# Kernel tuning notes

Measured on AMD Instinct MI355X. Metric: run time of the kernel, lower is better.

The kernel has to match this reference:

```python
import jax, jax.numpy as jnp
import numpy as np

B = 8192       # batch
HID = 1024     # hidden_dim
HEADS = 8      # head_count
OBS, ACT, N_AGENTS = 128, 32, 4
ENC_IN = N_AGENTS * OBS + ACT   # 544
DEC_IN = (N_AGENTS - 1) * ACT   # 96


def _linear(key, fan_in, fan_out):
    k1, k2 = jax.random.split(key)
    lim = 1.0 / np.sqrt(fan_in)
    W = jax.random.uniform(k1, (fan_in, fan_out), minval=-lim, maxval=lim, dtype=jnp.float32)
    b = jax.random.uniform(k2, (fan_out,), minval=-lim, maxval=lim, dtype=jnp.float32)
    return W, b


def setup_inputs() -> dict:
    key = jax.random.key(0)
    ks = jax.random.split(key, 10)
    s = jax.random.normal(ks[0], (B, N_AGENTS * OBS), dtype=jnp.float32)
    a = jax.random.normal(ks[1], (B, N_AGENTS * ACT), dtype=jnp.float32)
    W_enc_in, b_enc_in = _linear(ks[2], ENC_IN, HID)   # encoder_input_fc
    W_dec_in, b_dec_in = _linear(ks[3], DEC_IN, HID)   # decoder_input_fc
    W_eh, b_eh = _linear(ks[4], HID, HID)              # fc_encoder_input
    head_ks = jax.random.split(ks[5], HEADS)
    Wb = [_linear(k, HID, HID) for k in head_ks]       # fc_encoder_heads
    W_heads = jnp.stack([w for w, _ in Wb], axis=0)    # [H, HID, HID]
    b_heads = jnp.stack([b for _, b in Wb], axis=0)    # [H, HID]
    W_dh, b_dh = _linear(ks[6], HID, HID)              # fc_decoder_input
    W1, b1 = _linear(ks[7], HID, HID)                  # fc1
    W2, b2 = _linear(ks[8], HID, 1)                    # fc2
    return {"s": s, "a": a,
            "W_enc_in": W_enc_in, "b_enc_in": b_enc_in,
            "W_dec_in": W_dec_in, "b_dec_in": b_dec_in,
            "W_eh": W_eh, "b_eh": b_eh,
            "W_heads": W_heads, "b_heads": b_heads,
            "W_dh": W_dh, "b_dh": b_dh,
            "W1": W1, "b1": b1, "W2": W2, "b2": b2}


def reference(s, a, W_enc_in, b_enc_in, W_dec_in, b_dec_in, W_eh, b_eh,
              W_heads, b_heads, W_dh, b_dh, W1, b1, W2, b2):
    relu = jax.nn.relu
    # agent id = 0: own action is a[:, :ACT], others' actions are a[:, ACT:]
    enc_input = jnp.concatenate([s, a[:, :ACT]], axis=1) @ W_enc_in + b_enc_in   # [B, HID]
    dec_input = a[:, ACT:] @ W_dec_in + b_dec_in                                 # [B, HID]
    # Attention_ATT_2
    encoder_h = relu(enc_input @ W_eh + b_eh)                                    # [B, HID]
    encoder_heads = relu(jnp.einsum('bd,hde->hbe', encoder_h, W_heads)
                         + b_heads[:, None, :])                                  # [H, B, HID]
    decoder_H = relu(dec_input @ W_dh + b_dh)                                    # [B, HID]
    scores = jnp.einsum('hbd,bd->bh', encoder_heads, decoder_H)                  # [B, H]
    attn = jax.nn.softmax(scores, axis=1)                                        # [B, H]
    context = jnp.einsum('hbd,bh->bd', encoder_heads, attn)                      # [B, HID]
    x = relu(context @ W1 + b1)
    q = x @ W2 + b2                                                              # [B, 1]
    return q
```

## Files before the change

### kernel.cpp

```cpp
#include <hip/hip_runtime.h>
#include <hip/hip_bf16.h>
#include <hip/hip_fp16.h>

#define BATCH   8192
#define HID     1024
#define HEADS   8
#define BC      2048

typedef unsigned int  u32;
typedef unsigned short u16;
typedef __attribute__((ext_vector_type(8))) short bf16x8;
typedef __attribute__((ext_vector_type(4))) float f32x4;

__device__ __forceinline__ u32 pack_hi2(u32 u0, u32 u1) {
    return (u0 >> 16) | (u1 & 0xFFFF0000u);
}
__device__ __forceinline__ void split1(float x, u16& h, u16& l) {
    const u32 u = __float_as_uint(x);
    h = (u16)(u >> 16);
    const float r = x - __uint_as_float(u & 0xFFFF0000u);
    l = (u16)(__float_as_uint(r) >> 16);
}
__device__ __forceinline__ void splitA4(float4 v, uint2& hi, uint2& lo) {
    u32 u0 = __float_as_uint(v.x), u1 = __float_as_uint(v.y),
        u2 = __float_as_uint(v.z), u3 = __float_as_uint(v.w);
    float r0 = v.x - __uint_as_float(u0 & 0xFFFF0000u);
    float r1 = v.y - __uint_as_float(u1 & 0xFFFF0000u);
    float r2 = v.z - __uint_as_float(u2 & 0xFFFF0000u);
    float r3 = v.w - __uint_as_float(u3 & 0xFFFF0000u);
    hi.x = pack_hi2(u0, u1);
    hi.y = pack_hi2(u2, u3);
    lo.x = pack_hi2(__float_as_uint(r0), __float_as_uint(r1));
    lo.y = pack_hi2(__float_as_uint(r2), __float_as_uint(r3));
}

__device__ __forceinline__ void gld16(const u16* g, u16* l) {
    __builtin_amdgcn_global_load_lds(
        (const __attribute__((address_space(1))) u32*)g,
        (__attribute__((address_space(3))) u32*)l, 16, 0, 0);
}

struct WSplitArgs {
    const float* src[6];
    u16* hi[6];
    u16* lo[6];
};

__global__ __launch_bounds__(256) void split_weight_all(WSplitArgs args)
{
    const int z = blockIdx.z;
    int which, zz = 0;
    if (z < 3)       { which = z; }
    else if (z < 11) { which = 3; zz = z - 3; }
    else             { which = z - 7; }
    const int KT = (which == 4) ? 17 : (which == 5 ? 3 : 32);
    const int kt = blockIdx.x;
    if (kt >= KT) return;
    const int K = KT * 32;
    const long long zoff = (long long)zz * K * 1024;
    const float* W  = args.src[which] + zoff;
    u16* hi = args.hi[which] + zoff;
    u16* lo = args.lo[which] + zoff;

    const int n0  = blockIdx.y * 128;
    const int tid = threadIdx.x;
    const int k   = tid >> 3;
    const int ng  = (tid & 7) * 16;
    const float* src = W + (long long)(kt * 32 + k) * 1024 + n0 + ng;
    u16* dh = hi + ((long long)kt * 1024 + n0) * 32 + k;
    u16* dl = lo + ((long long)kt * 1024 + n0) * 32 + k;
#pragma unroll
    for (int t = 0; t < 4; t++) {
        const float4 v = *(const float4*)(src + t * 4);
        u16 h0, l0, h1, l1, h2, l2, h3, l3;
        split1(v.x, h0, l0); split1(v.y, h1, l1);
        split1(v.z, h2, l2); split1(v.w, h3, l3);
        const int nb = (ng + t * 4) * 32;
        dh[nb]      = h0; dl[nb]      = l0;
        dh[nb + 32] = h1; dl[nb + 32] = l1;
        dh[nb + 64] = h2; dl[nb + 64] = l2;
        dh[nb + 96] = h3; dl[nb + 96] = l3;
    }
}

#define MFMA_Q(IB, JB) \
    __builtin_amdgcn_s_setprio(1); \
    _Pragma("unroll") \
    for (int i_ = 0; i_ < 4; i_++) \
        _Pragma("unroll") \
        for (int j_ = 0; j_ < 2; j_++) \
            acc[(IB) + i_][(JB) + j_] = __builtin_amdgcn_mfma_f32_16x16x32_bf16(ah[i_], bh[(JB) + j_], acc[(IB) + i_][(JB) + j_], 0, 0, 0); \
    _Pragma("unroll") \
    for (int i_ = 0; i_ < 4; i_++) \
        _Pragma("unroll") \
        for (int j_ = 0; j_ < 2; j_++) \
            acc[(IB) + i_][(JB) + j_] = __builtin_amdgcn_mfma_f32_16x16x32_bf16(ah[i_], bl[(JB) + j_], acc[(IB) + i_][(JB) + j_], 0, 0, 0); \
    _Pragma("unroll") \
    for (int i_ = 0; i_ < 4; i_++) \
        _Pragma("unroll") \
        for (int j_ = 0; j_ < 2; j_++) \
            acc[(IB) + i_][(JB) + j_] = __builtin_amdgcn_mfma_f32_16x16x32_bf16(al[i_], bh[(JB) + j_], acc[(IB) + i_][(JB) + j_], 0, 0, 0); \
    __builtin_amdgcn_s_setprio(0);

#define SBAR() \
    __builtin_amdgcn_s_barrier(); \
    __builtin_amdgcn_sched_barrier(0);

#define G_GEOM \
    const int tid  = threadIdx.x; \
    const int lane = tid & 63; \
    const int wv   = tid >> 6; \
    const int wm   = wv >> 1, wn = wv & 1; \
    const int fr   = lane & 15; \
    const int fq   = lane >> 4; \
    const int m0   = blockIdx.y * 256; \
    const int n0   = blockIdx.x * 128; \
    const int lro2 = (lane >> 2) * 32 + (((lane & 3) ^ ((lane >> 3) & 3)) * 8); \
    const int fqx2 = (fq ^ ((fr >> 1) & 3)) * 8; \
    const int wrA  = wv * 32; \
    const int wrB  = wv * 16;

#define G_STAGE_A(buf_, t_) { \
    u16* d_ = (buf_); \
    const long long ao_ = abase + (long long)(t_) * astep; \
    gld16(Ahp + ao_ + (long long)wrA * 32 + lro2, d_ + wrA * 32); \
    gld16(Ahp + ao_ + (long long)(wrA + 16) * 32 + lro2, d_ + (wrA + 16) * 32); \
    gld16(Alp + ao_ + (long long)wrA * 32 + lro2, d_ + 8192 + wrA * 32); \
    gld16(Alp + ao_ + (long long)(wrA + 16) * 32 + lro2, d_ + 8192 + (wrA + 16) * 32); }

#define G_STAGE_B(buf_, t_) { \
    u16* d_ = (buf_); \
    const long long bo_ = bbase + (long long)(t_) * 32768; \
    gld16(Bhp + bo_ + (long long)wrB * 32 + lro2, d_ + 16384 + wrB * 32); \
    gld16(Blp + bo_ + (long long)wrB * 32 + lro2, d_ + 20480 + wrB * 32); }

#define G_RD_A(bp_) \
    _Pragma("unroll") \
    for (int i_ = 0; i_ < 4; i_++) { \
        const int off_ = (wm * 64 + i_ * 16 + fr) * 32 + fqx2; \
        ah[i_] = *(const bf16x8*)((bp_) + off_); \
        al[i_] = *(const bf16x8*)((bp_) + 8192 + off_); }

#define G_RD_B(bp_, JB) \
    _Pragma("unroll") \
    for (int j_ = 0; j_ < 2; j_++) { \
        const int off_ = (wn * 64 + ((JB) + j_) * 16 + fr) * 32 + fqx2; \
        bh[(JB) + j_] = *(const bf16x8*)((bp_) + 16384 + off_); \
        bl[(JB) + j_] = *(const bf16x8*)((bp_) + 20480 + off_); }

#define G_LOOP \
    const int KT = K >> 5; \
    const long long astep = (long long)MA * 32; \
    const long long abase = ((long long)moff + m0) * 32; \
    const long long bbase = (long long)n0 * 32; \
    G_STAGE_A(smem, 0); G_STAGE_B(smem, 0); \
    G_STAGE_A(smem + 24576, 1); G_STAGE_B(smem + 24576, 1); \
    asm volatile("s_waitcnt vmcnt(6)" ::: "memory"); \
    SBAR() \
    for (int t = 0; t < KT; t++) { \
        const u16* bp = smem + (t % 3) * 24576; \
        u16* nb = smem + ((t + 2) % 3) * 24576; \
        const bool more = (t + 2 < KT); \
        bf16x8 ah[4], al[4], bh[4], bl[4]; \
        G_RD_A(bp) \
        G_RD_B(bp, 0) \
        if (more) G_STAGE_A(nb, t + 2); \
        __builtin_amdgcn_sched_barrier(0); \
        MFMA_Q(0, 0) \
        SBAR() \
        G_RD_B(bp, 2) \
        if (more) G_STAGE_B(nb, t + 2); \
        __builtin_amdgcn_sched_barrier(0); \
        MFMA_Q(0, 2) \
        if (more) { asm volatile("s_waitcnt vmcnt(6)" ::: "memory"); } \
        else      { asm volatile("s_waitcnt vmcnt(0)" ::: "memory"); } \
        SBAR() \
    }

template <int RELU, int OUTP>
__global__ __launch_bounds__(512, 2) void gemm_fast(
    const u16* __restrict__ Ahp, const u16* __restrict__ Alp, int MA, int moff,
    const u16* __restrict__ Bhp, const u16* __restrict__ Blp,
    const float* __restrict__ bias,
    float* __restrict__ Cf,
    u16* __restrict__ Chp, u16* __restrict__ Clp, int MC,
    int K)
{
    __shared__ alignas(16) u16 smem[3 * 24576];
    G_GEOM

    f32x4 acc[4][4];
#pragma unroll
    for (int i = 0; i < 4; i++)
#pragma unroll
        for (int j = 0; j < 4; j++) acc[i][j] = 0;

    G_LOOP

#pragma unroll
    for (int j = 0; j < 4; j++) {
        const int n = n0 + wn * 64 + j * 16 + fr;
        const float bb = bias[n];
#pragma unroll
        for (int i = 0; i < 4; i++) {
#pragma unroll
            for (int r = 0; r < 4; r++) {
                const int m = m0 + wm * 64 + i * 16 + fq * 4 + r;
                float v = acc[i][j][r] + bb;
                if (RELU) v = fmaxf(v, 0.0f);
                if (OUTP) {
                    u16 h, l;
                    split1(v, h, l);
                    const long long d = ((long long)(n >> 5) * MC + moff + m) * 32 + (n & 31);
                    Chp[d] = h;
                    Clp[d] = l;
                } else {
                    Cf[(long long)m * 1024 + n] = v;
                }
            }
        }
    }
}

#define H_STAGE_A(buf_, t_) { \
    u16* d_ = (buf_); \
    const long long ao_ = abase + (long long)(t_) * astep; \
    gld16(Ahp + ao_ + (long long)wrA * 32 + lro2, d_ + wrA * 32); \
    gld16(Ahp + ao_ + (long long)(wrA + 16) * 32 + lro2, d_ + (wrA + 16) * 32); \
    gld16(Alp + ao_ + (long long)wrA * 32 + lro2, d_ + 8192 + wrA * 32); \
    gld16(Alp + ao_ + (long long)(wrA + 16) * 32 + lro2, d_ + 8192 + (wrA + 16) * 32); }

#define H_STAGE_B(buf_, t_) { \
    u16* d_ = (buf_); \
    const long long bo_ = bbase + (long long)(t_) * 32768; \
    gld16(Bhp + bo_ + (long long)wrA * 32 + lro2, d_ + 16384 + wrA * 32); \
    gld16(Bhp + bo_ + (long long)(wrA + 16) * 32 + lro2, d_ + 16384 + (wrA + 16) * 32); \
    gld16(Blp + bo_ + (long long)wrA * 32 + lro2, d_ + 24576 + wrA * 32); \
    gld16(Blp + bo_ + (long long)(wrA + 16) * 32 + lro2, d_ + 24576 + (wrA + 16) * 32); }

#define H_RD_A(bp_, RB) \
    _Pragma("unroll") \
    for (int i_ = 0; i_ < 4; i_++) { \
        const int off_ = ((RB) + i_ * 16 + fr) * 32 + fqx2; \
        ah[i_] = *(const bf16x8*)((bp_) + off_); \
        al[i_] = *(const bf16x8*)((bp_) + 8192 + off_); }

#define H_RD_B(bp_, JB) \
    _Pragma("unroll") \
    for (int j_ = 0; j_ < 2; j_++) { \
        const int off_ = (wn * 64 + ((JB) + j_) * 16 + fr) * 32 + fqx2; \
        bh[(JB) + j_] = *(const bf16x8*)((bp_) + 16384 + off_); \
        bl[(JB) + j_] = *(const bf16x8*)((bp_) + 24576 + off_); }

__global__ __launch_bounds__(512, 2) void heads_kernel(
    const u16* __restrict__ Ahp, const u16* __restrict__ Alp, int MA, int moff,
    const u16* __restrict__ Whp, const u16* __restrict__ Wlp,
    const float* __restrict__ b_heads,
    const float* __restrict__ decH,
    __half* __restrict__ headsb,
    float* __restrict__ scoresp)
{
    __shared__ alignas(16) u16 smem[2 * 32768];
    __shared__ float scred[4][256];
    const int tid  = threadIdx.x;
    const int lane = tid & 63;
    const int wv   = tid >> 6;
    const int wm   = wv >> 2;
    const int wn   = wv & 3;
    const int fr   = lane & 15;
    const int fq   = lane >> 4;
    const int m0   = blockIdx.y * 256;
    const int n0   = blockIdx.x * 256;
    const int lro2 = (lane >> 2) * 32 + (((lane & 3) ^ ((lane >> 3) & 3)) * 8);
    const int fqx2 = (fq ^ ((fr >> 1) & 3)) * 8;
    const int wrA  = wv * 32;
    const int h = blockIdx.z;
    const u16* Bhp = Whp + (long long)h * 1048576;
    const u16* Blp = Wlp + (long long)h * 1048576;
    const float* bias = b_heads + h * 1024;

    f32x4 acc[8][4];
#pragma unroll
    for (int i = 0; i < 8; i++)
#pragma unroll
        for (int j = 0; j < 4; j++) acc[i][j] = 0;

    const long long astep = (long long)MA * 32;
    const long long abase = ((long long)moff + m0) * 32;
    const long long bbase = (long long)n0 * 32;

    H_STAGE_A(smem, 0);
    H_STAGE_B(smem, 0);
    asm volatile("s_waitcnt vmcnt(0)" ::: "memory");
    SBAR()

    for (int t = 0; t < 32; t++) {
        const u16* bp = smem + (t & 1) * 32768;
        u16* nb = smem + ((t + 1) & 1) * 32768;
        const bool more = (t + 1 < 32);
        bf16x8 ah[4], al[4], bh[4], bl[4];
        H_RD_A(bp, wm * 128)
        H_RD_B(bp, 0)
        if (more) H_STAGE_A(nb, t + 1);
        __builtin_amdgcn_sched_barrier(0);
        MFMA_Q(0, 0)
        SBAR()
        H_RD_B(bp, 2)
        if (more) H_STAGE_B(nb, t + 1);
        __builtin_amdgcn_sched_barrier(0);
        MFMA_Q(0, 2)
        SBAR()
        H_RD_A(bp, wm * 128 + 64)
        __builtin_amdgcn_sched_barrier(0);
        MFMA_Q(4, 0)
        SBAR()
        MFMA_Q(4, 2)
        asm volatile("s_waitcnt vmcnt(0)" ::: "memory");
        SBAR()
    }

    float part[8][4];
#pragma unroll
    for (int i = 0; i < 8; i++)
#pragma unroll
        for (int r = 0; r < 4; r++) part[i][r] = 0.0f;

#pragma unroll
    for (int j = 0; j < 4; j++) {
        const int n = n0 + wn * 64 + j * 16 + fr;
        const float bb = bias[n];
#pragma unroll
        for (int i = 0; i < 8; i++) {
#pragma unroll
            for (int r = 0; r < 4; r++) {
                const int b_loc = m0 + wm * 128 + i * 16 + fq * 4 + r;
                const float v = fmaxf(acc[i][j][r] + bb, 0.0f);
                headsb[((long long)b_loc * HEADS + h) * 1024 + n] = __float2half(v);
                part[i][r] = fmaf(v, decH[(long long)b_loc * 1024 + n], part[i][r]);
            }
        }
    }
#pragma unroll
    for (int off = 1; off < 16; off <<= 1)
#pragma unroll
        for (int i = 0; i < 8; i++)
#pragma unroll
            for (int r = 0; r < 4; r++)
                part[i][r] += __shfl_xor(part[i][r], off, 64);

    if (fr == 0) {
#pragma unroll
        for (int i = 0; i < 8; i++)
#pragma unroll
            for (int r = 0; r < 4; r++)
                scred[wn][wm * 128 + i * 16 + fq * 4 + r] = part[i][r];
    }
    __syncthreads();
    if (tid < 256) {
        const float sv = scred[0][tid] + scred[1][tid] + scred[2][tid] + scred[3][tid];
        scoresp[(long long)(h * 4 + blockIdx.x) * BC + m0 + tid] = sv;
    }
}

template <int RELU>
__global__ __launch_bounds__(256) void gemm_cvt(
    const float* __restrict__ src1, int lda1, int kofs1,
    const float* __restrict__ src2, int lda2, int ksplit,
    const u16* __restrict__ Bhp, const u16* __restrict__ Blp,
    const float* __restrict__ bias,
    u16* __restrict__ Chp, u16* __restrict__ Clp, int MC,
    int K)
{
    __shared__ alignas(16) u16 Ah[4096], Al[4096], Bh[4096], Bl[4096];
    const int tid  = threadIdx.x;
    const int lane = tid & 63;
    const int wv   = tid >> 6;
    const int wm   = wv >> 1, wn = wv & 1;
    const int fr   = lane & 15;
    const int fq   = lane >> 4;
    const int m0   = blockIdx.y * 128;
    const int n0   = blockIdx.x * 128;
    const int fqx  = (fq ^ (fr & 3)) * 8;
    const int lro  = (lane >> 2) * 32 + (((lane & 3) ^ ((lane >> 2) & 3)) * 8);
    const int br0  = wv * 16;
    const int br1  = 64 + wv * 16;
    const int ar   = tid >> 3;
    const int akq  = tid & 7;
    const int awoff = (((akq >> 1) ^ (ar & 3)) * 8) + (akq & 1) * 4;

    f32x4 acc[4][4];
#pragma unroll
    for (int i = 0; i < 4; i++)
#pragma unroll
        for (int j = 0; j < 4; j++) acc[i][j] = 0;

    const int KT = K >> 5;
    for (int kt = 0; kt < KT; kt++) {
        const int k0 = kt * 32;
        const float* srcp; int ldk, kc;
        if (k0 < ksplit) { srcp = src1; ldk = lda1; kc = k0 + kofs1; }
        else             { srcp = src2; ldk = lda2; kc = k0 - ksplit; }

        const u16* Bg  = Bhp + ((long long)kt * 1024 + n0) * 32;
        const u16* Bg2 = Blp + ((long long)kt * 1024 + n0) * 32;
        gld16(Bg  + br0 * 32 + lro, &Bh[br0 * 32]);
        gld16(Bg  + br1 * 32 + lro, &Bh[br1 * 32]);
        gld16(Bg2 + br0 * 32 + lro, &Bl[br0 * 32]);
        gld16(Bg2 + br1 * 32 + lro, &Bl[br1 * 32]);

#pragma unroll
        for (int it = 0; it < 4; it++) {
            const int row = ar + it * 32;
            const float4 v = *(const float4*)(srcp + (long long)(m0 + row) * ldk + kc + akq * 4);
            uint2 hi, lo;
            splitA4(v, hi, lo);
            *(uint2*)&Ah[row * 32 + awoff] = hi;
            *(uint2*)&Al[row * 32 + awoff] = lo;
        }
        __syncthreads();

        bf16x8 ah[4], al[4], bh[4], bl[4];
#pragma unroll
        for (int i = 0; i < 4; i++) {
            const int off = (wm * 64 + i * 16 + fr) * 32 + fqx;
            ah[i] = *(const bf16x8*)&Ah[off];
            al[i] = *(const bf16x8*)&Al[off];
        }
#pragma unroll
        for (int j = 0; j < 4; j++) {
            const int off = (wn * 64 + j * 16 + fr) * 32 + fqx;
            bh[j] = *(const bf16x8*)&Bh[off];
            bl[j] = *(const bf16x8*)&Bl[off];
        }
#pragma unroll
        for (int i = 0; i < 4; i++)
#pragma unroll
            for (int j = 0; j < 4; j++) {
                acc[i][j] = __builtin_amdgcn_mfma_f32_16x16x32_bf16(ah[i], bh[j], acc[i][j], 0, 0, 0);
                acc[i][j] = __builtin_amdgcn_mfma_f32_16x16x32_bf16(ah[i], bl[j], acc[i][j], 0, 0, 0);
                acc[i][j] = __builtin_amdgcn_mfma_f32_16x16x32_bf16(al[i], bh[j], acc[i][j], 0, 0, 0);
            }
        __syncthreads();
    }

#pragma unroll
    for (int j = 0; j < 4; j++) {
        const int n = n0 + wn * 64 + j * 16 + fr;
        const float bb = bias[n];
#pragma unroll
        for (int i = 0; i < 4; i++) {
#pragma unroll
            for (int r = 0; r < 4; r++) {
                const int m = m0 + wm * 64 + i * 16 + fq * 4 + r;
                float v = acc[i][j][r] + bb;
                if (RELU) v = fmaxf(v, 0.0f);
                u16 h, l;
                split1(v, h, l);
                const long long d = ((long long)(n >> 5) * MC + m) * 32 + (n & 31);
                Chp[d] = h;
                Clp[d] = l;
            }
        }
    }
}

__global__ __launch_bounds__(256) void context_kernel(
    const __half* __restrict__ headsb, const float* __restrict__ scoresp,
    u16* __restrict__ ctx_hi, u16* __restrict__ ctx_lo, int MC, int row0)
{
    __shared__ float sc_s[32];
    __shared__ float attn_s[HEADS];
    const int b = blockIdx.x;
    const int tid = threadIdx.x;
    if (tid < 32) sc_s[tid] = scoresp[(long long)tid * BC + b];
    __syncthreads();
    if (tid == 0) {
        float sc[HEADS];
#pragma unroll
        for (int h = 0; h < HEADS; h++) {
            float s = 0.0f;
#pragma unroll
            for (int nt = 0; nt < 4; nt++) s += sc_s[h * 4 + nt];
            sc[h] = s;
        }
        float mx = sc[0];
#pragma unroll
        for (int h = 1; h < HEADS; h++) mx = fmaxf(mx, sc[h]);
        float e[HEADS], sum = 0.0f;
#pragma unroll
        for (int h = 0; h < HEADS; h++) { e[h] = __expf(sc[h] - mx); sum += e[h]; }
        const float inv = 1.0f / sum;
#pragma unroll
        for (int h = 0; h < HEADS; h++) attn_s[h] = e[h] * inv;
    }
    __syncthreads();

    const int d = tid * 4;
    float w[HEADS];
#pragma unroll
    for (int h = 0; h < HEADS; h++) w[h] = attn_s[h];
    float4 acc = make_float4(0.f, 0.f, 0.f, 0.f);
#pragma unroll
    for (int h = 0; h < HEADS; h++) {
        const __half2* hp = (const __half2*)(headsb + ((long long)b * HEADS + h) * 1024 + d);
        const float2 f0 = __half22float2(hp[0]);
        const float2 f1 = __half22float2(hp[1]);
        acc.x = fmaf(w[h], f0.x, acc.x);
        acc.y = fmaf(w[h], f0.y, acc.y);
        acc.z = fmaf(w[h], f1.x, acc.z);
        acc.w = fmaf(w[h], f1.y, acc.w);
    }
    uint2 hi, lo;
    splitA4(acc, hi, lo);
    const long long off = ((long long)(d >> 5) * MC + row0 + b) * 32 + (d & 31);
    *(uint2*)(ctx_hi + off) = hi;
    *(uint2*)(ctx_lo + off) = lo;
}

__global__ __launch_bounds__(256) void fc2_kernel(
    const float* __restrict__ x, const float* __restrict__ W2,
    const float* __restrict__ b2, float* __restrict__ q)
{
    const int b   = blockIdx.x;
    const int tid = threadIdx.x;
    __shared__ float red[4];

    const float4 xv = *(const float4*)(x + (long long)b * 1024 + tid * 4);
    const float4 wv = *(const float4*)(W2 + tid * 4);
    float p = xv.x * wv.x + xv.y * wv.y + xv.z * wv.z + xv.w * wv.w;
#pragma unroll
    for (int off = 32; off > 0; off >>= 1) p += __shfl_down(p, off, 64);
    if ((tid & 63) == 0) red[tid >> 6] = p;
    __syncthreads();
    if (tid == 0) q[b] = red[0] + red[1] + red[2] + red[3] + b2[0];
}

extern "C" void kernel_launch(void* const* d_in, const int* in_sizes, int n_in,
                              void* d_out, int out_size, void* d_ws, size_t ws_size,
                              hipStream_t stream)
{
    const float* s        = (const float*)d_in[0];
    const float* a        = (const float*)d_in[1];
    const float* W_enc_in = (const float*)d_in[2];
    const float* b_enc_in = (const float*)d_in[3];
    const float* W_dec_in = (const float*)d_in[4];
    const float* b_dec_in = (const float*)d_in[5];
    const float* W_eh     = (const float*)d_in[6];
    const float* b_eh     = (const float*)d_in[7];
    const float* W_heads  = (const float*)d_in[8];
    const float* b_heads  = (const float*)d_in[9];
    const float* W_dh     = (const float*)d_in[10];
    const float* b_dh     = (const float*)d_in[11];
    const float* W1       = (const float*)d_in[12];
    const float* b1       = (const float*)d_in[13];
    const float* W2       = (const float*)d_in[14];
    const float* b2       = (const float*)d_in[15];
    float* q_out = (float*)d_out;

    u16* P = (u16*)d_ws;
    u16* enc_hi = P; P += 557056;
    u16* enc_lo = P; P += 557056;
    u16* dec_hi = P; P += 98304;
    u16* dec_lo = P; P += 98304;
    u16* eh_hi  = P; P += 1048576;
    u16* eh_lo  = P; P += 1048576;
    u16* dh_hi  = P; P += 1048576;
    u16* dh_lo  = P; P += 1048576;
    u16* w1_hi  = P; P += 1048576;
    u16* w1_lo  = P; P += 1048576;
    u16* wh_hi  = P; P += 8388608;
    u16* wh_lo  = P; P += 8388608;
    char* act = (char*)P;

    const dim3 blk(256);
    const dim3 blk512(512);

    WSplitArgs wa;
    wa.src[0] = W_eh;    wa.hi[0] = eh_hi;  wa.lo[0] = eh_lo;
    wa.src[1] = W_dh;    wa.hi[1] = dh_hi;  wa.lo[1] = dh_lo;
    wa.src[2] = W1;      wa.hi[2] = w1_hi;  wa.lo[2] = w1_lo;
    wa.src[3] = W_heads; wa.hi[3] = wh_hi;  wa.lo[3] = wh_lo;
    wa.src[4] = W_enc_in; wa.hi[4] = enc_hi; wa.lo[4] = enc_lo;
    wa.src[5] = W_dec_in; wa.hi[5] = dec_hi; wa.lo[5] = dec_lo;
    split_weight_all<<<dim3(32, 8, 13), blk, 0, stream>>>(wa);

    const bool high = (ws_size >= 150011904ULL);

    if (high) {
        u16*    bufA_hi = (u16*)act;
        u16*    bufA_lo = bufA_hi + 8388608;
        __half* headsb  = (__half*)act;
        u16*    encH_hi = (u16*)(act + 33554432);
        u16*    encH_lo = encH_hi + 8388608;
        float*  decH    = (float*)(act + 2LL * 33554432);
        float*  scoresp = (float*)(act + 3LL * 33554432);

        const dim3 ggc(8, 64, 1);
        const dim3 ggf(8, 32, 1);
        gemm_cvt<0><<<ggc, blk, 0, stream>>>(s, 512, 0, a, 128, 512,
            enc_hi, enc_lo, b_enc_in, bufA_hi, bufA_lo, 8192, 544);
        gemm_fast<1, 1><<<ggf, blk512, 0, stream>>>(bufA_hi, bufA_lo, 8192, 0,
            eh_hi, eh_lo, b_eh, nullptr, encH_hi, encH_lo, 8192, 1024);
        gemm_cvt<0><<<ggc, blk, 0, stream>>>(a, 128, 32, a, 128, 1 << 28,
            dec_hi, dec_lo, b_dec_in, bufA_hi, bufA_lo, 8192, 96);
        gemm_fast<1, 0><<<ggf, blk512, 0, stream>>>(bufA_hi, bufA_lo, 8192, 0,
            dh_hi, dh_lo, b_dh, decH, nullptr, nullptr, 0, 1024);

        for (int c = 0; c < BATCH / BC; c++) {
            heads_kernel<<<dim3(4, BC / 256, 8), blk512, 0, stream>>>(
                encH_hi, encH_lo, 8192, c * BC, wh_hi, wh_lo, b_heads,
                decH + (long long)c * BC * 1024, headsb, scoresp);
            context_kernel<<<dim3(BC), blk, 0, stream>>>(
                headsb, scoresp, encH_hi, encH_lo, 8192, c * BC);
        }
        gemm_fast<1, 0><<<ggf, blk512, 0, stream>>>(encH_hi, encH_lo, 8192, 0,
            w1_hi, w1_lo, b1, decH, nullptr, nullptr, 0, 1024);
        fc2_kernel<<<dim3(BATCH), blk, 0, stream>>>(decH, W2, b2, q_out);
    } else {
        __half* headsb  = (__half*)act;
        u16*    bufA_hi = (u16*)act;
        u16*    bufA_lo = bufA_hi + 2097152;
        u16*    encH_hi = (u16*)(act + 33554432);
        u16*    encH_lo = encH_hi + 2097152;
        float*  decH    = (float*)(act + 33554432 + 8388608);
        float*  scoresp = (float*)(act + 33554432 + 2LL * 8388608);

        const dim3 ggc(8, BC / 128, 1);
        const dim3 ggf(8, BC / 256, 1);
        for (int c = 0; c < BATCH / BC; c++) {
            const float* sC = s + (long long)c * BC * 512;
            const float* aC = a + (long long)c * BC * 128;
            gemm_cvt<0><<<ggc, blk, 0, stream>>>(sC, 512, 0, aC, 128, 512,
                enc_hi, enc_lo, b_enc_in, bufA_hi, bufA_lo, BC, 544);
            gemm_fast<1, 1><<<ggf, blk512, 0, stream>>>(bufA_hi, bufA_lo, BC, 0,
                eh_hi, eh_lo, b_eh, nullptr, encH_hi, encH_lo, BC, 1024);
            gemm_cvt<0><<<ggc, blk, 0, stream>>>(aC, 128, 32, aC, 128, 1 << 28,
                dec_hi, dec_lo, b_dec_in, bufA_hi, bufA_lo, BC, 96);
            gemm_fast<1, 0><<<ggf, blk512, 0, stream>>>(bufA_hi, bufA_lo, BC, 0,
                dh_hi, dh_lo, b_dh, decH, nullptr, nullptr, 0, 1024);
            heads_kernel<<<dim3(4, BC / 256, 8), blk512, 0, stream>>>(
                encH_hi, encH_lo, BC, 0, wh_hi, wh_lo, b_heads,
                decH, headsb, scoresp);
            context_kernel<<<dim3(BC), blk, 0, stream>>>(
                headsb, scoresp, encH_hi, encH_lo, BC, 0);
            gemm_fast<1, 0><<<ggf, blk512, 0, stream>>>(encH_hi, encH_lo, BC, 0,
                w1_hi, w1_lo, b1, decH, nullptr, nullptr, 0, 1024);
            fc2_kernel<<<dim3(BC), blk, 0, stream>>>(decH, W2, b2, q_out + (long long)c * BC);
        }
    }
}
```

Measured before the change: 751.3 us.

## Double-buffer A fragments in registers and cut per-iteration barriers in GEMM loops

Reworks the K-loops of both the generic GEMM and the heads kernel so the next tile's A/B fragments are read from LDS into a second register set while the current tile's MFMAs run. The heads kernel goes from four workgroup barriers per iteration to one, with explicit lgkmcnt/vmcnt waits before it. The generic GEMM is unrolled by two tiles and alternates register sets. This aims to hide LDS read latency and barrier stalls behind MFMA work, at the cost of more VGPRs, which may pressure occupancy under the 512x2 launch bounds. The two-tile unroll assumes an even tile count, so K values giving an odd KT may run an extra tile.

```diff
diff --git a/kernel.cpp b/kernel.cpp
--- a/kernel.cpp
+++ b/kernel.cpp
@@ -39,6 +39,8 @@
         (const __attribute__((address_space(1))) u32*)g,
         (__attribute__((address_space(3))) u32*)l, 16, 0, 0);
 }
+
+#define SCHED0 __builtin_amdgcn_sched_barrier(0)
 
 struct WSplitArgs {
     const float* src[6];
@@ -83,38 +85,34 @@
     }
 }
 
-#define MFMA_Q(IB, JB) \
+#define MFMA_Q24(AH_, AL_, IB, JB) \
     __builtin_amdgcn_s_setprio(1); \
     _Pragma("unroll") \
     for (int i_ = 0; i_ < 4; i_++) \
         _Pragma("unroll") \
         for (int j_ = 0; j_ < 2; j_++) \
-            acc[(IB) + i_][(JB) + j_] = __builtin_amdgcn_mfma_f32_16x16x32_bf16(ah[i_], bh[(JB) + j_], acc[(IB) + i_][(JB) + j_], 0, 0, 0); \
+            acc[(IB) + i_][(JB) + j_] = __builtin_amdgcn_mfma_f32_16x16x32_bf16(AH_[i_], bh[(JB) + j_], acc[(IB) + i_][(JB) + j_], 0, 0, 0); \
     _Pragma("unroll") \
     for (int i_ = 0; i_ < 4; i_++) \
         _Pragma("unroll") \
         for (int j_ = 0; j_ < 2; j_++) \
-            acc[(IB) + i_][(JB) + j_] = __builtin_amdgcn_mfma_f32_16x16x32_bf16(ah[i_], bl[(JB) + j_], acc[(IB) + i_][(JB) + j_], 0, 0, 0); \
+            acc[(IB) + i_][(JB) + j_] = __builtin_amdgcn_mfma_f32_16x16x32_bf16(AH_[i_], bl[(JB) + j_], acc[(IB) + i_][(JB) + j_], 0, 0, 0); \
     _Pragma("unroll") \
     for (int i_ = 0; i_ < 4; i_++) \
         _Pragma("unroll") \
         for (int j_ = 0; j_ < 2; j_++) \
-            acc[(IB) + i_][(JB) + j_] = __builtin_amdgcn_mfma_f32_16x16x32_bf16(al[i_], bh[(JB) + j_], acc[(IB) + i_][(JB) + j_], 0, 0, 0); \
+            acc[(IB) + i_][(JB) + j_] = __builtin_amdgcn_mfma_f32_16x16x32_bf16(AL_[i_], bh[(JB) + j_], acc[(IB) + i_][(JB) + j_], 0, 0, 0); \
     __builtin_amdgcn_s_setprio(0);
-
-#define SBAR() \
-    __builtin_amdgcn_s_barrier(); \
-    __builtin_amdgcn_sched_barrier(0);
 
 #define G_GEOM \
     const int tid  = threadIdx.x; \
     const int lane = tid & 63; \
     const int wv   = tid >> 6; \
     const int wm   = wv >> 1, wn = wv & 1; \
+    const int m0   = blockIdx.y * 256; \
+    const int n0   = blockIdx.x * 128; \
     const int fr   = lane & 15; \
     const int fq   = lane >> 4; \
-    const int m0   = blockIdx.y * 256; \
-    const int n0   = blockIdx.x * 128; \
     const int lro2 = (lane >> 2) * 32 + (((lane & 3) ^ ((lane >> 3) & 3)) * 8); \
     const int fqx2 = (fq ^ ((fr >> 1) & 3)) * 8; \
     const int wrA  = wv * 32; \
@@ -134,12 +132,12 @@
     gld16(Bhp + bo_ + (long long)wrB * 32 + lro2, d_ + 16384 + wrB * 32); \
     gld16(Blp + bo_ + (long long)wrB * 32 + lro2, d_ + 20480 + wrB * 32); }
 
-#define G_RD_A(bp_) \
+#define G_RD_A(AH_, AL_, bp_) \
     _Pragma("unroll") \
     for (int i_ = 0; i_ < 4; i_++) { \
         const int off_ = (wm * 64 + i_ * 16 + fr) * 32 + fqx2; \
-        ah[i_] = *(const bf16x8*)((bp_) + off_); \
-        al[i_] = *(const bf16x8*)((bp_) + 8192 + off_); }
+        AH_[i_] = *(const bf16x8*)((bp_) + off_); \
+        AL_[i_] = *(const bf16x8*)((bp_) + 8192 + off_); }
 
 #define G_RD_B(bp_, JB) \
     _Pragma("unroll") \
@@ -148,34 +146,26 @@
         bh[(JB) + j_] = *(const bf16x8*)((bp_) + 16384 + off_); \
         bl[(JB) + j_] = *(const bf16x8*)((bp_) + 20480 + off_); }
 
-#define G_LOOP \
-    const int KT = K >> 5; \
-    const long long astep = (long long)MA * 32; \
-    const long long abase = ((long long)moff + m0) * 32; \
-    const long long bbase = (long long)n0 * 32; \
-    G_STAGE_A(smem, 0); G_STAGE_B(smem, 0); \
-    G_STAGE_A(smem + 24576, 1); G_STAGE_B(smem + 24576, 1); \
-    asm volatile("s_waitcnt vmcnt(6)" ::: "memory"); \
-    SBAR() \
-    for (int t = 0; t < KT; t++) { \
-        const u16* bp = smem + (t % 3) * 24576; \
-        u16* nb = smem + ((t + 2) % 3) * 24576; \
-        const bool more = (t + 2 < KT); \
-        bf16x8 ah[4], al[4], bh[4], bl[4]; \
-        G_RD_A(bp) \
-        G_RD_B(bp, 0) \
-        if (more) G_STAGE_A(nb, t + 2); \
-        __builtin_amdgcn_sched_barrier(0); \
-        MFMA_Q(0, 0) \
-        SBAR() \
-        G_RD_B(bp, 2) \
-        if (more) G_STAGE_B(nb, t + 2); \
-        __builtin_amdgcn_sched_barrier(0); \
-        MFMA_Q(0, 2) \
-        if (more) { asm volatile("s_waitcnt vmcnt(6)" ::: "memory"); } \
-        else      { asm volatile("s_waitcnt vmcnt(0)" ::: "memory"); } \
-        SBAR() \
-    }
+#define G_TILE(t_, AH_, AL_, NAH_, NAL_) { \
+    const u16* bp = smem + ((t_) % 3) * 24576; \
+    u16* nb2 = smem + (((t_) + 2) % 3) * 24576; \
+    const u16* np = smem + (((t_) + 1) % 3) * 24576; \
+    const bool s_ = (t_) + 2 < KT; \
+    const bool p_ = (t_) + 1 < KT; \
+    G_RD_B(bp, 2) \
+    if (s_) { G_STAGE_A(nb2, (t_) + 2); G_STAGE_B(nb2, (t_) + 2); } \
+    SCHED0; \
+    MFMA_Q24(AH_, AL_, 0, 0) \
+    asm volatile("s_waitcnt lgkmcnt(0)" ::: "memory"); \
+    if (s_) { asm volatile("s_waitcnt vmcnt(6)" ::: "memory"); } \
+    else    { asm volatile("s_waitcnt vmcnt(0)" ::: "memory"); } \
+    __builtin_amdgcn_s_barrier(); \
+    SCHED0; \
+    if (p_) { G_RD_A(NAH_, NAL_, np) G_RD_B(np, 0) } \
+    SCHED0; \
+    MFMA_Q24(AH_, AL_, 0, 2) \
+    SCHED0; \
+}
 
 template <int RELU, int OUTP>
 __global__ __launch_bounds__(512, 2) void gemm_fast(
@@ -195,7 +185,25 @@
 #pragma unroll
         for (int j = 0; j < 4; j++) acc[i][j] = 0;
 
-    G_LOOP
+    const int KT = K >> 5;
+    const long long astep = (long long)MA * 32;
+    const long long abase = ((long long)moff + m0) * 32;
+    const long long bbase = (long long)n0 * 32;
+
+    bf16x8 ahA[4], alA[4], ahB[4], alB[4], bh[4], bl[4];
+
+    G_STAGE_A(smem, 0); G_STAGE_B(smem, 0);
+    G_STAGE_A(smem + 24576, 1); G_STAGE_B(smem + 24576, 1);
+    asm volatile("s_waitcnt vmcnt(6)" ::: "memory");
+    __builtin_amdgcn_s_barrier();
+    SCHED0;
+    G_RD_A(ahA, alA, smem)
+    G_RD_B(smem, 0)
+
+    for (int t = 0; t < KT; t += 2) {
+        G_TILE(t,     ahA, alA, ahB, alB)
+        G_TILE(t + 1, ahB, alB, ahA, alA)
+    }
 
 #pragma unroll
     for (int j = 0; j < 4; j++) {
@@ -238,19 +246,33 @@
     gld16(Blp + bo_ + (long long)wrA * 32 + lro2, d_ + 24576 + wrA * 32); \
     gld16(Blp + bo_ + (long long)(wrA + 16) * 32 + lro2, d_ + 24576 + (wrA + 16) * 32); }
 
-#define H_RD_A(bp_, RB) \
+#define H_RD_A0(bp_) \
     _Pragma("unroll") \
     for (int i_ = 0; i_ < 4; i_++) { \
-        const int off_ = ((RB) + i_ * 16 + fr) * 32 + fqx2; \
-        ah[i_] = *(const bf16x8*)((bp_) + off_); \
-        al[i_] = *(const bf16x8*)((bp_) + 8192 + off_); }
-
-#define H_RD_B(bp_, JB) \
+        const int off_ = (wm * 128 + i_ * 16 + fr) * 32 + fqx2; \
+        ah0[i_] = *(const bf16x8*)((bp_) + off_); \
+        al0[i_] = *(const bf16x8*)((bp_) + 8192 + off_); }
+
+#define H_RD_A1(bp_) \
+    _Pragma("unroll") \
+    for (int i_ = 0; i_ < 4; i_++) { \
+        const int off_ = (wm * 128 + 64 + i_ * 16 + fr) * 32 + fqx2; \
+        ah1[i_] = *(const bf16x8*)((bp_) + off_); \
+        al1[i_] = *(const bf16x8*)((bp_) + 8192 + off_); }
+
+#define H_RD_B01(bp_) \
     _Pragma("unroll") \
     for (int j_ = 0; j_ < 2; j_++) { \
-        const int off_ = (wn * 64 + ((JB) + j_) * 16 + fr) * 32 + fqx2; \
-        bh[(JB) + j_] = *(const bf16x8*)((bp_) + 16384 + off_); \
-        bl[(JB) + j_] = *(const bf16x8*)((bp_) + 24576 + off_); }
+        const int off_ = (wn * 64 + j_ * 16 + fr) * 32 + fqx2; \
+        bh[j_] = *(const bf16x8*)((bp_) + 16384 + off_); \
+        bl[j_] = *(const bf16x8*)((bp_) + 24576 + off_); }
+
+#define H_RD_B23(bp_) \
+    _Pragma("unroll") \
+    for (int j_ = 0; j_ < 2; j_++) { \
+        const int off_ = (wn * 64 + (2 + j_) * 16 + fr) * 32 + fqx2; \
+        bh[2 + j_] = *(const bf16x8*)((bp_) + 16384 + off_); \
+        bl[2 + j_] = *(const bf16x8*)((bp_) + 24576 + off_); }
 
 __global__ __launch_bounds__(512, 2) void heads_kernel(
     const u16* __restrict__ Ahp, const u16* __restrict__ Alp, int MA, int moff,
@@ -289,34 +311,39 @@
     const long long abase = ((long long)moff + m0) * 32;
     const long long bbase = (long long)n0 * 32;
 
+    bf16x8 ah0[4], al0[4], ah1[4], al1[4], bh[4], bl[4];
+
     H_STAGE_A(smem, 0);
     H_STAGE_B(smem, 0);
     asm volatile("s_waitcnt vmcnt(0)" ::: "memory");
-    SBAR()
+    __builtin_amdgcn_s_barrier();
+    SCHED0;
+    H_RD_A0(smem)
+    H_RD_B01(smem)
 
     for (int t = 0; t < 32; t++) {
         const u16* bp = smem + (t & 1) * 32768;
         u16* nb = smem + ((t + 1) & 1) * 32768;
-        const bool more = (t + 1 < 32);
-        bf16x8 ah[4], al[4], bh[4], bl[4];
-        H_RD_A(bp, wm * 128)
-        H_RD_B(bp, 0)
+        const bool more = t < 31;
+        H_RD_B23(bp)
         if (more) H_STAGE_A(nb, t + 1);
-        __builtin_amdgcn_sched_barrier(0);
-        MFMA_Q(0, 0)
-        SBAR()
-        H_RD_B(bp, 2)
+        SCHED0;
+        MFMA_Q24(ah0, al0, 0, 0)
+        SCHED0;
+        H_RD_A1(bp)
         if (more) H_STAGE_B(nb, t + 1);
-        __builtin_amdgcn_sched_barrier(0);
-        MFMA_Q(0, 2)
-        SBAR()
-        H_RD_A(bp, wm * 128 + 64)
-        __builtin_amdgcn_sched_barrier(0);
-        MFMA_Q(4, 0)
-        SBAR()
-        MFMA_Q(4, 2)
+        SCHED0;
+        MFMA_Q24(ah0, al0, 0, 2)
+        SCHED0;
+        MFMA_Q24(ah1, al1, 4, 0)
+        asm volatile("s_waitcnt lgkmcnt(0)" ::: "memory");
         asm volatile("s_waitcnt vmcnt(0)" ::: "memory");
-        SBAR()
+        __builtin_amdgcn_s_barrier();
+        SCHED0;
+        if (more) { H_RD_A0(nb) H_RD_B01(nb) }
+        SCHED0;
+        MFMA_Q24(ah1, al1, 4, 2)
+        SCHED0;
     }
 
     float part[8][4];
```

After: 712.4 us. 1.05x faster.
